# Kernel optimization log

Measured on AMD Instinct MI355X. Metric: run time of the kernel, lower is better.

Reference implementation:

```python
import jax, jax.numpy as jnp
import numpy as np

PI = 3.14159265358979323846
MARGIN = 6.0
DIM = 256
ENT_TOT = 43234
REL_RANGE = (6.0 + 2.0) / DIM  # (margin + epsilon) / dim = 0.03125


def setup_inputs() -> dict:
    key = jax.random.key(0)
    k1, k2, k3 = jax.random.split(key, 3)
    head = jax.random.normal(k1, (32, 2 * DIM), dtype=jnp.float32)
    relation = jax.random.normal(k2, (32, DIM), dtype=jnp.float32)
    ent_emb = jax.random.normal(k3, (ENT_TOT, 2 * DIM), dtype=jnp.float32)
    return {"head": head, "relation": relation, "ent_emb": ent_emb}


def reference(head, relation, ent_emb):
    # head: (B, 2D) -> re/im halves (B, D)
    re_h, im_h = jnp.split(head, 2, axis=-1)
    # entity table: (E, 2D) -> (E, D) each
    re_t, im_t = jnp.split(ent_emb, 2, axis=-1)
    # phase rotation from relation embedding
    phase = relation / (REL_RANGE / PI)          # (B, D)
    re_r = jnp.cos(phase)
    im_r = jnp.sin(phase)
    # complex rotation of head by relation: (B, D)
    re_rot = re_h * re_r - im_h * im_r
    im_rot = re_h * im_r + im_h * re_r
    # difference against every entity, broadcast to (B, E, D)
    re_s = re_rot[:, None, :] - re_t[None, :, :]
    im_s = im_rot[:, None, :] - im_t[None, :, :]
    # L2 norm over the complex pair, summed over D -> (B, E)
    dist = jnp.sqrt(re_s * re_s + im_s * im_s).sum(axis=-1)
    return MARGIN - dist
```

## Files before the change

kernel.cpp:

```cpp
#include <hip/hip_runtime.h>
#include <math.h>

#define DIMH 256
#define NB   32
#define E_TOT 43234
#define TE_B 16
#define TE_C 2
#define PHASE_DIV 0.009947183943243459f

typedef float v2f __attribute__((ext_vector_type(2)));

__global__ __launch_bounds__(256) void rot_kernel(const float* __restrict__ head,
                                                  const float* __restrict__ rel,
                                                  float4* __restrict__ rot_v4) {
    int i  = blockIdx.x * 256 + threadIdx.x;
    int b  = i >> 7;
    int dp = i & 127;
    int d0 = dp * 2;
    float4 w;
    {
        float re_h = head[b * 2 * DIMH + d0];
        float im_h = head[b * 2 * DIMH + DIMH + d0];
        float s, c;
        sincosf(rel[b * DIMH + d0] / PHASE_DIV, &s, &c);
        w.x = re_h * c - im_h * s;
        w.z = re_h * s + im_h * c;
    }
    {
        float re_h = head[b * 2 * DIMH + d0 + 1];
        float im_h = head[b * 2 * DIMH + DIMH + d0 + 1];
        float s, c;
        sincosf(rel[b * DIMH + d0 + 1] / PHASE_DIV, &s, &c);
        w.y = re_h * c - im_h * s;
        w.w = re_h * s + im_h * c;
    }
    rot_v4[b * (DIMH / 2) + dp] = w;
}

__device__ __forceinline__ v2f sqrt2(v2f s) {
    v2f r;
    r.x = __builtin_amdgcn_sqrtf(s.x);
    r.y = __builtin_amdgcn_sqrtf(s.y);
    return r;
}

__device__ __forceinline__ float dpp_reduce32(float h) {
    h += __int_as_float(__builtin_amdgcn_update_dpp(0, __float_as_int(h), 0x111, 0xf, 0xf, true));
    h += __int_as_float(__builtin_amdgcn_update_dpp(0, __float_as_int(h), 0x112, 0xf, 0xf, true));
    h += __int_as_float(__builtin_amdgcn_update_dpp(0, __float_as_int(h), 0x114, 0xf, 0xf, true));
    h += __int_as_float(__builtin_amdgcn_update_dpp(0, __float_as_int(h), 0x118, 0xf, 0xf, true));
    h += __int_as_float(__builtin_amdgcn_update_dpp(0, __float_as_int(h), 0x142, 0xf, 0xf, true));
    return h;
}

__global__ __launch_bounds__(256, 4) void dist_kernel(const float* __restrict__ ent,
                                                      const float4* __restrict__ rot_v4,
                                                      float* __restrict__ out) {
    __shared__ float2 s_e[TE_C][8][32];

    const int tid = threadIdx.x;
    const int ds  = tid & 31;
    const int bg  = tid >> 5;
    const int eb  = blockIdx.x * TE_B;

    v2f rr[4][4], ri[4][4];
    #pragma unroll
    for (int jj = 0; jj < 4; ++jj) {
        const int b = bg * 4 + jj;
        #pragma unroll
        for (int p = 0; p < 4; ++p) {
            float4 w = rot_v4[b * (DIMH / 2) + ds * 4 + p];
            rr[jj][p].x = w.x; rr[jj][p].y = w.y;
            ri[jj][p].x = w.z; ri[jj][p].y = w.w;
        }
    }

    const int e_l   = tid >> 7;
    const int plane = (tid >> 6) & 1;
    const int qd    = tid & 63;

    float4 pf;
    auto load_chunk = [&](int ch) {
        int eg = min(eb + ch * TE_C + e_l, E_TOT - 1);
        pf = *reinterpret_cast<const float4*>(&ent[(size_t)eg * (2 * DIMH) + plane * DIMH + 4 * qd]);
    };

    load_chunk(0);

    for (int ch = 0; ch < TE_B / TE_C; ++ch) {
        {
            const int dsw = qd >> 1;
            const int u0  = ((qd & 1) ? 2 : 0) + plane * 4;
            float2 lo, hi;
            lo.x = pf.x; lo.y = pf.y;
            hi.x = pf.z; hi.y = pf.w;
            s_e[e_l][u0][dsw]     = lo;
            s_e[e_l][u0 + 1][dsw] = hi;
        }
        __syncthreads();

        if (ch + 1 < TE_B / TE_C) load_chunk(ch + 1);

        v2f acc[4][TE_C];
        #pragma unroll
        for (int jj = 0; jj < 4; ++jj)
            #pragma unroll
            for (int ee = 0; ee < TE_C; ++ee) { acc[jj][ee].x = 0.f; acc[jj][ee].y = 0.f; }

        #pragma unroll
        for (int ee = 0; ee < TE_C; ++ee) {
            v2f er[4], ei[4];
            #pragma unroll
            for (int p = 0; p < 4; ++p) {
                float2 a = s_e[ee][p][ds];
                float2 b = s_e[ee][p + 4][ds];
                er[p].x = a.x; er[p].y = a.y;
                ei[p].x = b.x; ei[p].y = b.y;
            }
            #pragma unroll
            for (int jj = 0; jj < 4; ++jj)
                #pragma unroll
                for (int p = 0; p < 4; ++p) {
                    v2f a = rr[jj][p] - er[p];
                    v2f b = ri[jj][p] - ei[p];
                    acc[jj][ee] += sqrt2(a * a + b * b);
                }
        }
        __syncthreads();

        #pragma unroll
        for (int jj = 0; jj < 4; ++jj)
            #pragma unroll
            for (int ee = 0; ee < TE_C; ++ee) {
                float h = dpp_reduce32(acc[jj][ee].x + acc[jj][ee].y);
                const int e = eb + ch * TE_C + ee;
                if ((tid & 31) == 31 && e < E_TOT)
                    out[(size_t)(bg * 4 + jj) * E_TOT + e] = 6.0f - h;
            }
    }
}

extern "C" void kernel_launch(void* const* d_in, const int* in_sizes, int n_in,
                              void* d_out, int out_size, void* d_ws, size_t ws_size,
                              hipStream_t stream) {
    const float* head = (const float*)d_in[0];
    const float* rel  = (const float*)d_in[1];
    const float* ent  = (const float*)d_in[2];
    float4* rot_v4 = (float4*)d_ws;

    rot_kernel<<<(NB * DIMH / 2) / 256, 256, 0, stream>>>(head, rel, rot_v4);

    int eblocks = (E_TOT + TE_B - 1) / TE_B;
    dist_kernel<<<eblocks, 256, 0, stream>>>(ent, rot_v4, (float*)d_out);
}
```

Measured before the change: 176.3 us.

## Replace LDS-staged entity tiles with per-thread register double-buffered global loads

Drops the shared-memory staging of entity rows and both block barriers; each thread now loads its own slice of the entity's real and imaginary parts directly into registers with a one-entity prefetch. Blocks process 32 entities one at a time, and launch bounds drop to 3 waves per SIMD to leave register room. The trade is redundant global loads across the 8 waves of a block, served by cache, instead of LDS reuse.

```diff
diff --git a/kernel.cpp b/kernel.cpp
--- a/kernel.cpp
+++ b/kernel.cpp
@@ -4,11 +4,11 @@
 #define DIMH 256
 #define NB   32
 #define E_TOT 43234
-#define TE_B 16
-#define TE_C 2
+#define EPB  32
 #define PHASE_DIV 0.009947183943243459f
 
 typedef float v2f __attribute__((ext_vector_type(2)));
+typedef float v4f __attribute__((ext_vector_type(4)));
 
 __global__ __launch_bounds__(256) void rot_kernel(const float* __restrict__ head,
                                                   const float* __restrict__ rel,
@@ -53,15 +53,13 @@
     return h;
 }
 
-__global__ __launch_bounds__(256, 4) void dist_kernel(const float* __restrict__ ent,
+__global__ __launch_bounds__(256, 3) void dist_kernel(const float* __restrict__ ent,
                                                       const float4* __restrict__ rot_v4,
                                                       float* __restrict__ out) {
-    __shared__ float2 s_e[TE_C][8][32];
-
     const int tid = threadIdx.x;
     const int ds  = tid & 31;
     const int bg  = tid >> 5;
-    const int eb  = blockIdx.x * TE_B;
+    const int eb  = blockIdx.x * EPB;
 
     v2f rr[4][4], ri[4][4];
     #pragma unroll
@@ -75,68 +73,48 @@
         }
     }
 
-    const int e_l   = tid >> 7;
-    const int plane = (tid >> 6) & 1;
-    const int qd    = tid & 63;
-
-    float4 pf;
-    auto load_chunk = [&](int ch) {
-        int eg = min(eb + ch * TE_C + e_l, E_TOT - 1);
-        pf = *reinterpret_cast<const float4*>(&ent[(size_t)eg * (2 * DIMH) + plane * DIMH + 4 * qd]);
+    v4f cur[4], nxt[4];
+    auto load_e = [&](int e, v4f* buf) {
+        e = min(e, E_TOT - 1);
+        const float* b = &ent[(size_t)e * (2 * DIMH) + ds * 8];
+        buf[0] = *reinterpret_cast<const v4f*>(b);
+        buf[1] = *reinterpret_cast<const v4f*>(b + 4);
+        buf[2] = *reinterpret_cast<const v4f*>(b + DIMH);
+        buf[3] = *reinterpret_cast<const v4f*>(b + DIMH + 4);
     };
 
-    load_chunk(0);
+    load_e(eb, cur);
 
-    for (int ch = 0; ch < TE_B / TE_C; ++ch) {
-        {
-            const int dsw = qd >> 1;
-            const int u0  = ((qd & 1) ? 2 : 0) + plane * 4;
-            float2 lo, hi;
-            lo.x = pf.x; lo.y = pf.y;
-            hi.x = pf.z; hi.y = pf.w;
-            s_e[e_l][u0][dsw]     = lo;
-            s_e[e_l][u0 + 1][dsw] = hi;
-        }
-        __syncthreads();
+    for (int i = 0; i < EPB; ++i) {
+        if (i + 1 < EPB) load_e(eb + i + 1, nxt);
 
-        if (ch + 1 < TE_B / TE_C) load_chunk(ch + 1);
+        v2f er[4], ei[4];
+        er[0] = cur[0].xy; er[1] = cur[0].zw; er[2] = cur[1].xy; er[3] = cur[1].zw;
+        ei[0] = cur[2].xy; ei[1] = cur[2].zw; ei[2] = cur[3].xy; ei[3] = cur[3].zw;
 
-        v2f acc[4][TE_C];
+        v2f acc[4];
         #pragma unroll
-        for (int jj = 0; jj < 4; ++jj)
-            #pragma unroll
-            for (int ee = 0; ee < TE_C; ++ee) { acc[jj][ee].x = 0.f; acc[jj][ee].y = 0.f; }
+        for (int jj = 0; jj < 4; ++jj) { acc[jj].x = 0.f; acc[jj].y = 0.f; }
 
         #pragma unroll
-        for (int ee = 0; ee < TE_C; ++ee) {
-            v2f er[4], ei[4];
+        for (int p = 0; p < 4; ++p)
             #pragma unroll
-            for (int p = 0; p < 4; ++p) {
-                float2 a = s_e[ee][p][ds];
-                float2 b = s_e[ee][p + 4][ds];
-                er[p].x = a.x; er[p].y = a.y;
-                ei[p].x = b.x; ei[p].y = b.y;
+            for (int jj = 0; jj < 4; ++jj) {
+                v2f a = rr[jj][p] - er[p];
+                v2f b = ri[jj][p] - ei[p];
+                acc[jj] += sqrt2(a * a + b * b);
             }
-            #pragma unroll
-            for (int jj = 0; jj < 4; ++jj)
-                #pragma unroll
-                for (int p = 0; p < 4; ++p) {
-                    v2f a = rr[jj][p] - er[p];
-                    v2f b = ri[jj][p] - ei[p];
-                    acc[jj][ee] += sqrt2(a * a + b * b);
-                }
+
+        const int e = eb + i;
+        #pragma unroll
+        for (int jj = 0; jj < 4; ++jj) {
+            float h = dpp_reduce32(acc[jj].x + acc[jj].y);
+            if ((tid & 31) == 31 && e < E_TOT)
+                out[(size_t)(bg * 4 + jj) * E_TOT + e] = 6.0f - h;
         }
-        __syncthreads();
 
         #pragma unroll
-        for (int jj = 0; jj < 4; ++jj)
-            #pragma unroll
-            for (int ee = 0; ee < TE_C; ++ee) {
-                float h = dpp_reduce32(acc[jj][ee].x + acc[jj][ee].y);
-                const int e = eb + ch * TE_C + ee;
-                if ((tid & 31) == 31 && e < E_TOT)
-                    out[(size_t)(bg * 4 + jj) * E_TOT + e] = 6.0f - h;
-            }
+        for (int q = 0; q < 4; ++q) cur[q] = nxt[q];
     }
 }
 
@@ -150,6 +128,6 @@
 
     rot_kernel<<<(NB * DIMH / 2) / 256, 256, 0, stream>>>(head, rel, rot_v4);
 
-    int eblocks = (E_TOT + TE_B - 1) / TE_B;
+    int eblocks = (E_TOT + EPB - 1) / EPB;
     dist_kernel<<<eblocks, 256, 0, stream>>>(ent, rot_v4, (float*)d_out);
 }
```

Result: slower. 195.1 us (+10.6%).
